# Optimization experiments

Measured on AMD Instinct MI355X. Metric: run time of the kernel, lower is better.

The kernel has to match this reference:

```python
import jax, jax.numpy as jnp
import numpy as np

D = 2        # NUM_DIM (spatial/velocity dimension)
B = 64       # number of (r, r') query pairs
P = 512      # num coefficient positions
NV = 64      # num velocity quadrature points
NC = 1       # num coefficient channels (sigma)
H = 64       # attention MLP hidden width
TW = 128     # transport MLP width
DEPTH = 3    # res_block_depth


def setup_inputs() -> dict:
    key = jax.random.key(0)
    ks = jax.random.split(key, 20)
    rnd = lambda i, shape, s=1.0: (s * jax.random.normal(ks[i], shape, dtype=jnp.float32))
    uni = lambda i, shape: jax.random.uniform(ks[i], shape, dtype=jnp.float32)
    return dict(
        coords=rnd(0, (B, 2 * D)),
        coords_prime=rnd(1, (B, 2 * D)),
        scattering_kernel=uni(2, (B, NV)),
        position_coords=rnd(3, (P, D)),
        sigma=uni(4, (P, NC)),
        velocity_coords=rnd(5, (NV, D)),
        velocity_weights=uni(6, (NV,)),
        self_scattering_kernel=uni(7, (NV, NV)),
        aW0=rnd(8, (2 * D + 2, H), (2 * D + 2) ** -0.5), ab0=jnp.zeros((H,), jnp.float32),
        aW1=rnd(9, (H, H), H ** -0.5), ab1=jnp.zeros((H,), jnp.float32),
        aW2=rnd(10, (H, 1), H ** -0.5), ab2=jnp.zeros((1,), jnp.float32),
        tW0=rnd(11, (4 * D + NC, TW), (4 * D + NC) ** -0.5), tb0=jnp.zeros((TW,), jnp.float32),
        tW1=rnd(12, (TW, TW), TW ** -0.5), tb1=jnp.zeros((TW,), jnp.float32),
        tW2=rnd(13, (TW, TW), TW ** -0.5), tb2=jnp.zeros((TW,), jnp.float32),
        rW=rnd(14, (DEPTH - 1, TW, TW), TW ** -0.5), rb=jnp.zeros((DEPTH - 1, TW), jnp.float32),
        fW=rnd(15, (TW, 1), TW ** -0.5), fb=jnp.zeros((1,), jnp.float32),
    )


def _coeff(x, v, pos, vals, aW0, ab0, aW1, ab1, aW2, ab2):
    # x, v: (..., D); pos: (P, D); vals: (P, NC)
    coords = jnp.concatenate([x, v], axis=-1)                          # (..., 2D)
    ang_g = v / jnp.sqrt(jnp.sum(v * v, axis=-1, keepdims=True) + 1e-16)
    rel = x[..., None, :] - pos                                        # (..., P, D)
    rd = jnp.sqrt(jnp.sum(rel * rel, axis=-1) + 1e-16)                 # (..., P)
    pl = jnp.einsum('...pd,...d->...p', rel, ang_g)                    # positions_local
    al = pl / (rd + 1e-8)                                              # angles_local
    frames = jnp.stack([al, pl], axis=-1)                              # (..., P, 2)
    q = jnp.broadcast_to(coords[..., None, :], frames.shape[:-1] + (coords.shape[-1],))
    qk = jnp.concatenate([q, frames], axis=-1)                         # (..., P, 2D+2)
    h = jax.nn.relu(qk @ aW0 + ab0)
    h = jax.nn.relu(h @ aW1 + ab1)
    logits = (h @ aW2 + ab2)[..., 0]                                   # (..., P)
    logits = jnp.where(pl > 0, logits, -1e30)
    attw = jax.nn.softmax(logits, axis=-1)
    attn = jnp.einsum('...p,pc->...c', attw, vals)                     # (..., NC)
    return jnp.exp(-attn)


def _transport(x, v, xp, vp, pos, vals,
               aW0, ab0, aW1, ab1, aW2, ab2, tW0, tb0, tW1, tb1, tW2, tb2):
    coeff = _coeff(x, v, pos, vals, aW0, ab0, aW1, ab1, aW2, ab2)
    inp = jnp.concatenate([x, v, xp, vp, coeff], axis=-1)              # (..., 4D+NC)
    h = jax.nn.relu(inp @ tW0 + tb0)
    h = jax.nn.relu(h @ tW1 + tb1)
    h = jax.nn.relu(h @ tW2 + tb2)                                     # activate_final=True
    return jnp.exp(h)                                                  # (..., TW)


def _forward(coords, coords_prime, scattering_kernel, position_coords, sigma,
             velocity_coords, velocity_weights, self_scattering_kernel,
             aW0, ab0, aW1, ab1, aW2, ab2, tW0, tb0, tW1, tb1, tW2, tb2,
             rW, rb, fW, fb):
    x, v = coords[:, :D], coords[:, D:]
    xp, vp = coords_prime[:, :D], coords_prime[:, D:]
    mlp_p = (aW0, ab0, aW1, ab1, aW2, ab2, tW0, tb0, tW1, tb1, tW2, tb2)
    # direct transport term: (B, TW)
    g = _transport(x, v, xp, vp, position_coords, sigma, *mlp_p)
    # scatter model: vmap over velocity_coords -> (B, NV, TW)
    b = coords.shape[0]
    vB = jnp.broadcast_to(velocity_coords, (b, NV, D))
    xB = jnp.broadcast_to(x[:, None, :], (b, NV, D))
    xpB = jnp.broadcast_to(xp[:, None, :], (b, NV, D))
    vpB = jnp.broadcast_to(vp[:, None, :], (b, NV, D))
    cur = _transport(xB, vB, xpB, vpB, position_coords, sigma, *mlp_p)
    res_w = (1.0 - self_scattering_kernel) * velocity_weights          # (NV, NV)
    outs = [cur]
    for l in range(DEPTH - 1):  # layer_stack with per-layer params
        r = jnp.einsum('ij,bjw->biw', res_w, cur)
        r = jax.nn.relu(r @ rW[l] + rb[l])                             # MLP([TW]), activate_final
        cur = cur + r
        outs.append(cur)
    scat = jnp.stack(outs)                                             # (DEPTH, B, NV, TW)
    w = (1.0 - scattering_kernel) * velocity_weights                   # (B, NV)
    g = g + jnp.einsum('bj,dbjw->bw', w, scat)
    return g @ fW + fb                                                 # (B, 1)


def reference(coords, coords_prime, scattering_kernel, position_coords, sigma,
              velocity_coords, velocity_weights, self_scattering_kernel,
              aW0, ab0, aW1, ab1, aW2, ab2, tW0, tb0, tW1, tb1, tW2, tb2,
              rW, rb, fW, fb):
    return _forward(coords, coords_prime, scattering_kernel, position_coords, sigma,
                    velocity_coords, velocity_weights, self_scattering_kernel,
                    aW0, ab0, aW1, ab1, aW2, ab2, tW0, tb0, tW1, tb1, tW2, tb2,
                    rW, rb, fW, fb)
```

## Files before the change

kernel.cpp:

```cpp
#include <hip/hip_runtime.h>
#include <hip/hip_bf16.h>
#include <math.h>

#define D 2
#define B 64
#define P 512
#define NV 64
#define H 64
#define TW 128
#define NQ (B*NV + B)

typedef short short8 __attribute__((ext_vector_type(8)));
typedef short short4v __attribute__((ext_vector_type(4)));
typedef float f32x4 __attribute__((ext_vector_type(4)));
typedef int   int4v  __attribute__((ext_vector_type(4)));

static __device__ __forceinline__ unsigned short f2bf(float f) {
    unsigned int u = __builtin_bit_cast(unsigned int, f);
    u += 0x7FFFu + ((u >> 16) & 1u);
    return (unsigned short)(u >> 16);
}
static __device__ __forceinline__ unsigned int pk2bf(float a, float b) {
    __hip_bfloat162 h = __float22bfloat162_rn(make_float2(a, b));
    unsigned int u;
    __builtin_memcpy(&u, &h, 4);
    return u;
}

__global__ __launch_bounds__(256, 2) void coeff_kernel(
    const float* __restrict__ coords, const float* __restrict__ vel,
    const float* __restrict__ pos, const float* __restrict__ sigma,
    const float* __restrict__ aW0, const float* __restrict__ ab0,
    const float* __restrict__ aW1, const float* __restrict__ ab1,
    const float* __restrict__ aW2, const float* __restrict__ ab2,
    float* __restrict__ coeff_out)
{
    __shared__ unsigned short s_w1t[64*72];
    __shared__ float2 s_pos[P];
    __shared__ float  s_logit[2*P];

    const int tid  = threadIdx.x;
    const int lane = tid & 63, wid = tid >> 6;
    const int l15 = lane & 15, lg = lane >> 4;
    const int qi   = wid >> 1;
    const int half = wid & 1;
    const int q = blockIdx.x*2 + qi;

    for (int i = tid; i < H*H; i += 256) {
        const int k = i >> 6, n = i & 63;
        s_w1t[n*72 + k] = f2bf(aW1[i]);
    }
    {
        const float4 p4 = ((const float4*)pos)[tid];
        *(float4*)&s_pos[tid*2] = p4;
    }

    float x0, x1, v0, v1;
    {
        int b;
        if (q < B*NV) { b = q >> 6; const int j = q & 63;
            v0 = vel[2*j]; v1 = vel[2*j+1];
        } else { b = q - B*NV;
            v0 = coords[4*b+2]; v1 = coords[4*b+3];
        }
        x0 = coords[4*b]; x1 = coords[4*b+1];
    }
    const float rinv = rsqrtf(v0*v0 + v1*v1 + 1e-16f);
    const float a0 = v0*rinv, a1 = v1*rinv;

    float basev[16], w4v[16], w5v[16];
    #pragma unroll
    for (int jj = 0; jj < 16; ++jj) {
        const int k = lg*8 + (jj & 7) + (jj >> 3)*32;
        basev[jj] = ab0[k] + x0*aW0[k] + x1*aW0[64+k] + v0*aW0[128+k] + v1*aW0[192+k];
        w4v[jj]   = aW0[256+k];
        w5v[jj]   = aW0[320+k];
    }

    f32x4 b1v[4], w2v[4];
    #pragma unroll
    for (int nt = 0; nt < 4; ++nt) {
        const int n0 = nt*16 + lg*4;
        b1v[nt] = *(const f32x4*)&ab1[n0];
        w2v[nt] = *(const f32x4*)&aW2[n0];
    }
    __syncthreads();

    short8 afrag[4][2];
    #pragma unroll
    for (int nt = 0; nt < 4; ++nt)
        #pragma unroll
        for (int ks = 0; ks < 2; ++ks)
            afrag[nt][ks] = *(const short8*)&s_w1t[(nt*16 + l15)*72 + ks*32 + lg*8];

    #pragma unroll
    for (int jj = 0; jj < 16; ++jj)
        asm volatile("" : "+v"(basev[jj]), "+v"(w4v[jj]), "+v"(w5v[jj]));
    #pragma unroll
    for (int nt = 0; nt < 4; ++nt)
        asm volatile("" : "+v"(b1v[nt]), "+v"(w2v[nt]),
                          "+v"(afrag[nt][0]), "+v"(afrag[nt][1]));

    float pl, al;
    {
        const float2 p0v = s_pos[half*256 + l15];
        const float rx = x0 - p0v.x, ry = x1 - p0v.y;
        const float rd = __builtin_amdgcn_sqrtf(rx*rx + ry*ry + 1e-16f);
        pl = rx*a0 + ry*a1;
        al = __fdividef(pl, rd + 1e-8f);
    }
    for (int ps = 0; ps < 16; ++ps) {
        const int prow = half*256 + ps*16 + l15;
        float pln = pl, aln = al;
        if (ps < 15) {
            const float2 nxt = s_pos[prow + 16];
            const float rxn = x0 - nxt.x, ryn = x1 - nxt.y;
            const float rdn = __builtin_amdgcn_sqrtf(rxn*rxn + ryn*ryn + 1e-16f);
            pln = rxn*a0 + ryn*a1;
            aln = __fdividef(pln, rdn + 1e-8f);
        }

        int4v wlo, whi;
        #pragma unroll
        for (int jp = 0; jp < 4; ++jp) {
            const float t0 = fmaxf(fmaf(pl, w5v[2*jp],   fmaf(al, w4v[2*jp],   basev[2*jp])),   0.f);
            const float t1 = fmaxf(fmaf(pl, w5v[2*jp+1], fmaf(al, w4v[2*jp+1], basev[2*jp+1])), 0.f);
            const float u0 = fmaxf(fmaf(pl, w5v[8+2*jp],   fmaf(al, w4v[8+2*jp],   basev[8+2*jp])),   0.f);
            const float u1 = fmaxf(fmaf(pl, w5v[8+2*jp+1], fmaf(al, w4v[8+2*jp+1], basev[8+2*jp+1])), 0.f);
            wlo[jp] = (int)pk2bf(t0, t1);
            whi[jp] = (int)pk2bf(u0, u1);
        }
        const short8 bf0 = __builtin_bit_cast(short8, wlo);
        const short8 bf1 = __builtin_bit_cast(short8, whi);

        float ssum = 0.f;
        #pragma unroll
        for (int nt = 0; nt < 4; ++nt) {
            f32x4 acc = b1v[nt];
            acc = __builtin_amdgcn_mfma_f32_16x16x32_bf16(afrag[nt][0], bf0, acc, 0, 0, 0);
            acc = __builtin_amdgcn_mfma_f32_16x16x32_bf16(afrag[nt][1], bf1, acc, 0, 0, 0);
            ssum += fmaxf(acc[0], 0.f) * w2v[nt][0];
            ssum += fmaxf(acc[1], 0.f) * w2v[nt][1];
            ssum += fmaxf(acc[2], 0.f) * w2v[nt][2];
            ssum += fmaxf(acc[3], 0.f) * w2v[nt][3];
        }
        ssum += __shfl_xor(ssum, 16, 64);
        ssum += __shfl_xor(ssum, 32, 64);
        if (lane < 16) s_logit[qi*512 + prow] = (pl > 0.f) ? ssum : -1e30f;
        pl = pln; al = aln;
    }
    __syncthreads();

    const float* lgb = &s_logit[qi*512];
    const float4 l0 = *(const float4*)&lgb[lane*8];
    const float4 l1 = *(const float4*)&lgb[lane*8 + 4];
    float m = fmaxf(fmaxf(fmaxf(l0.x, l0.y), fmaxf(l0.z, l0.w)),
                    fmaxf(fmaxf(l1.x, l1.y), fmaxf(l1.z, l1.w)));
    #pragma unroll
    for (int o = 32; o > 0; o >>= 1) m = fmaxf(m, __shfl_xor(m, o, 64));

    const float4 g0 = *(const float4*)&sigma[lane*8];
    const float4 g1 = *(const float4*)&sigma[lane*8 + 4];
    float S = 0.f, T = 0.f, e;
    e = __expf(l0.x - m); S += e; T += e*g0.x;
    e = __expf(l0.y - m); S += e; T += e*g0.y;
    e = __expf(l0.z - m); S += e; T += e*g0.z;
    e = __expf(l0.w - m); S += e; T += e*g0.w;
    e = __expf(l1.x - m); S += e; T += e*g1.x;
    e = __expf(l1.y - m); S += e; T += e*g1.y;
    e = __expf(l1.z - m); S += e; T += e*g1.z;
    e = __expf(l1.w - m); S += e; T += e*g1.w;
    #pragma unroll
    for (int o = 32; o > 0; o >>= 1) { S += __shfl_xor(S, o, 64); T += __shfl_xor(T, o, 64); }
    if (lane == 0 && half == 0) coeff_out[q] = __expf(-(T / S));
}

__global__ __launch_bounds__(512) void transport_kernel(
    const float* __restrict__ coords, const float* __restrict__ coordsp,
    const float* __restrict__ vel,
    const float* __restrict__ tW0, const float* __restrict__ tb0,
    const float* __restrict__ tW1, const float* __restrict__ tb1,
    const float* __restrict__ tW2, const float* __restrict__ tb2,
    const float* __restrict__ coeff_ws, float* __restrict__ cur_ws,
    float* __restrict__ g_ws)
{
    __shared__ unsigned short s_w0t[128*40];
    __shared__ unsigned short s_wt[128*136];
    __shared__ unsigned short s_in[64*40];
    __shared__ unsigned short s_ha[64*136];
    __shared__ unsigned short s_hb[64*136];
    __shared__ float s_b[3*128];

    const int tid = threadIdx.x, g = blockIdx.x;
    const int lane = tid & 63, wid = tid >> 6;
    const int wm = wid & 3, wn = wid >> 2;
    const int l15 = lane & 15, lg = lane >> 4;
    const int irow = wm*16 + lg*4;
    const int qbase = g*64;

    for (int i = tid; i < 128*40; i += 512) {
        const int t = i / 40, k = i % 40;
        s_w0t[i] = (k < 9) ? f2bf(tW0[k*TW + t]) : 0;
    }
    for (int i = tid; i < 64*40; i += 512) s_in[i] = 0;
    {
        const int n = tid & 127, u0 = (tid >> 7)*4;
        #pragma unroll
        for (int k8 = 0; k8 < 8; ++k8) {
            const int u = u0 + 16*k8;
            short4v pk;
            #pragma unroll
            for (int c = 0; c < 4; ++c) pk[c] = (short)f2bf(tW1[(u+c)*TW + n]);
            *(short4v*)&s_wt[n*136 + u] = pk;
        }
    }
    if (tid < 128) { s_b[tid] = tb0[tid]; s_b[128+tid] = tb1[tid]; s_b[256+tid] = tb2[tid]; }
    __syncthreads();

    if (tid < 64) {
        const int q = qbase + tid;
        int b; float v0, v1;
        if (q < B*NV) { b = q >> 6; const int j = q & 63;
            v0 = vel[2*j]; v1 = vel[2*j+1];
        } else { b = q - B*NV;
            v0 = coords[4*b+2]; v1 = coords[4*b+3];
        }
        unsigned short* r = &s_in[tid*40];
        r[0] = f2bf(coords[4*b]);   r[1] = f2bf(coords[4*b+1]);
        r[2] = f2bf(v0);            r[3] = f2bf(v1);
        r[4] = f2bf(coordsp[4*b]);  r[5] = f2bf(coordsp[4*b+1]);
        r[6] = f2bf(coordsp[4*b+2]);r[7] = f2bf(coordsp[4*b+3]);
        r[8] = f2bf(coeff_ws[q]);
    }
    __syncthreads();

    {
        const short8 a0 = *(const short8*)&s_in[(wm*16 + l15)*40 + lg*8];
        #pragma unroll
        for (int nt = 0; nt < 4; ++nt) {
            const int col = wn*64 + nt*16 + l15;
            const short8 b0f = *(const short8*)&s_w0t[col*40 + lg*8];
            const float bias = s_b[col];
            f32x4 acc = { bias, bias, bias, bias };
            acc = __builtin_amdgcn_mfma_f32_16x16x32_bf16(a0, b0f, acc, 0, 0, 0);
            #pragma unroll
            for (int rg = 0; rg < 4; ++rg)
                s_ha[(irow + rg)*136 + col] = f2bf(fmaxf(acc[rg], 0.f));
        }
    }
    __syncthreads();

    {
        short8 af[4];
        #pragma unroll
        for (int ks = 0; ks < 4; ++ks)
            af[ks] = *(const short8*)&s_ha[(wm*16 + l15)*136 + ks*32 + lg*8];
        #pragma unroll
        for (int nt = 0; nt < 4; ++nt) {
            const int col = wn*64 + nt*16 + l15;
            const float bias = s_b[128 + col];
            f32x4 acc = { bias, bias, bias, bias };
            #pragma unroll
            for (int ks = 0; ks < 4; ++ks) {
                const short8 bfr = *(const short8*)&s_wt[col*136 + ks*32 + lg*8];
                acc = __builtin_amdgcn_mfma_f32_16x16x32_bf16(af[ks], bfr, acc, 0, 0, 0);
            }
            #pragma unroll
            for (int rg = 0; rg < 4; ++rg)
                s_hb[(irow + rg)*136 + col] = f2bf(fmaxf(acc[rg], 0.f));
        }
    }
    __syncthreads();

    {
        const int n = tid & 127, u0 = (tid >> 7)*4;
        #pragma unroll
        for (int k8 = 0; k8 < 8; ++k8) {
            const int u = u0 + 16*k8;
            short4v pk;
            #pragma unroll
            for (int c = 0; c < 4; ++c) pk[c] = (short)f2bf(tW2[(u+c)*TW + n]);
            *(short4v*)&s_wt[n*136 + u] = pk;
        }
    }
    __syncthreads();

    {
        short8 af[4];
        #pragma unroll
        for (int ks = 0; ks < 4; ++ks)
            af[ks] = *(const short8*)&s_hb[(wm*16 + l15)*136 + ks*32 + lg*8];
        #pragma unroll
        for (int nt = 0; nt < 4; ++nt) {
            const int col = wn*64 + nt*16 + l15;
            const float bias = s_b[256 + col];
            f32x4 acc = { bias, bias, bias, bias };
            #pragma unroll
            for (int ks = 0; ks < 4; ++ks) {
                const short8 bfr = *(const short8*)&s_wt[col*136 + ks*32 + lg*8];
                acc = __builtin_amdgcn_mfma_f32_16x16x32_bf16(af[ks], bfr, acc, 0, 0, 0);
            }
            #pragma unroll
            for (int rg = 0; rg < 4; ++rg) {
                const float o = __expf(fmaxf(acc[rg], 0.f));
                const int q = qbase + irow + rg;
                if (q < B*NV) cur_ws[q*TW + col] = o;
                else          g_ws[(q - B*NV)*TW + col] = o;
            }
        }
    }
}

__global__ __launch_bounds__(512) void scatter_kernel(
    const float* __restrict__ scat_k, const float* __restrict__ vw,
    const float* __restrict__ ssk,
    const float* __restrict__ rW, const float* __restrict__ rb,
    const float* __restrict__ fW, const float* __restrict__ fb,
    const float* __restrict__ cur_ws, const float* __restrict__ g_ws,
    float* __restrict__ out)
{
    __shared__ unsigned short s_At[128*72];
    __shared__ unsigned short s_r[64*136];
    __shared__ unsigned short s_rWt[128*136];
    __shared__ float s_wl[NV];
    __shared__ float s_fin[4*128];
    __shared__ float s_red[2];

    const int tid = threadIdx.x, b = blockIdx.x;
    const int lane = tid & 63, wid = tid >> 6;
    const int wm = wid & 3, wn = wid >> 2;
    const int l15 = lane & 15, lg = lane >> 4;
    const int irow = wm*16 + lg*4;

    if (tid < NV) s_wl[tid] = (1.f - scat_k[b*NV + tid]) * vw[tid];

    {
        const int w = tid & 127, j0 = tid >> 7;
        #pragma unroll
        for (int k = 0; k < 16; ++k) {
            const int j = j0 + 4*k;
            s_At[w*72 + j] = f2bf(cur_ws[(b*NV + j)*TW + w]);
        }
    }

    float areg[4][4], sreg[4][4];
    #pragma unroll
    for (int n = 0; n < 4; ++n) {
        const int wcol = wn*64 + n*16 + l15;
        #pragma unroll
        for (int rg = 0; rg < 4; ++rg) {
            const float v = cur_ws[(b*NV + irow + rg)*TW + wcol];
            areg[n][rg] = v; sreg[n][rg] = v;
        }
    }

    for (int l = 0; l < 2; ++l) {
        {
            const float* rWl = rW + l*TW*TW;
            const int w = tid & 127, u0 = (tid >> 7)*4;
            #pragma unroll
            for (int k = 0; k < 8; ++k) {
                const int u = u0 + 16*k;
                short4v pk;
                #pragma unroll
                for (int c = 0; c < 4; ++c) pk[c] = (short)f2bf(rWl[(u+c)*TW + w]);
                *(short4v*)&s_rWt[w*136 + u] = pk;
            }
        }
        __syncthreads();

        {
            short8 afrag[2];
            const int row = wm*16 + l15;
            #pragma unroll
            for (int ks = 0; ks < 2; ++ks) {
                const int k0 = ks*32 + lg*8;
                #pragma unroll
                for (int j = 0; j < 8; ++j) {
                    const float rv = (1.f - ssk[row*NV + k0 + j]) * vw[k0 + j];
                    afrag[ks][j] = (short)f2bf(rv);
                }
            }
            #pragma unroll
            for (int n = 0; n < 4; ++n) {
                const int col = wn*64 + n*16 + l15;
                f32x4 acc = {0.f, 0.f, 0.f, 0.f};
                #pragma unroll
                for (int ks = 0; ks < 2; ++ks) {
                    const short8 bfr = *(const short8*)&s_At[col*72 + ks*32 + lg*8];
                    acc = __builtin_amdgcn_mfma_f32_16x16x32_bf16(afrag[ks], bfr, acc, 0, 0, 0);
                }
                #pragma unroll
                for (int rg = 0; rg < 4; ++rg)
                    s_r[(irow + rg)*136 + col] = f2bf(acc[rg]);
            }
        }
        __syncthreads();

        {
            short8 af2[4];
            #pragma unroll
            for (int ks = 0; ks < 4; ++ks)
                af2[ks] = *(const short8*)&s_r[(wm*16 + l15)*136 + ks*32 + lg*8];
            #pragma unroll
            for (int n = 0; n < 4; ++n) {
                const int col = wn*64 + n*16 + l15;
                f32x4 acc = {0.f, 0.f, 0.f, 0.f};
                #pragma unroll
                for (int ks = 0; ks < 4; ++ks) {
                    const short8 bfr = *(const short8*)&s_rWt[col*136 + ks*32 + lg*8];
                    acc = __builtin_amdgcn_mfma_f32_16x16x32_bf16(af2[ks], bfr, acc, 0, 0, 0);
                }
                const float rbv = rb[l*TW + col];
                short4v pk;
                #pragma unroll
                for (int rg = 0; rg < 4; ++rg) {
                    areg[n][rg] += fmaxf(acc[rg] + rbv, 0.f);
                    sreg[n][rg] += areg[n][rg];
                    pk[rg] = (short)f2bf(areg[n][rg]);
                }
                *(short4v*)&s_At[col*72 + irow] = pk;
            }
        }
        __syncthreads();
    }

    float p[4];
    #pragma unroll
    for (int n = 0; n < 4; ++n) {
        float acc = 0.f;
        #pragma unroll
        for (int rg = 0; rg < 4; ++rg) acc += s_wl[irow + rg] * sreg[n][rg];
        acc += __shfl_xor(acc, 16, 64);
        acc += __shfl_xor(acc, 32, 64);
        p[n] = acc;
    }
    if (lg == 0) {
        #pragma unroll
        for (int n = 0; n < 4; ++n)
            s_fin[wm*128 + wn*64 + n*16 + l15] = p[n];
    }
    __syncthreads();

    if (tid < 128) {
        const int w = tid;
        const float tot = s_fin[w] + s_fin[128 + w] + s_fin[256 + w] + s_fin[384 + w];
        float pw = (g_ws[b*TW + w] + tot) * fW[w];
        #pragma unroll
        for (int o = 32; o > 0; o >>= 1) pw += __shfl_down(pw, o, 64);
        if ((tid & 63) == 0) s_red[tid >> 6] = pw;
    }
    __syncthreads();
    if (tid == 0) out[b] = s_red[0] + s_red[1] + fb[0];
}

extern "C" void kernel_launch(void* const* d_in, const int* in_sizes, int n_in,
                              void* d_out, int out_size, void* d_ws, size_t ws_size,
                              hipStream_t stream) {
    const float* coords  = (const float*)d_in[0];
    const float* coordsp = (const float*)d_in[1];
    const float* scatk   = (const float*)d_in[2];
    const float* pos     = (const float*)d_in[3];
    const float* sigma   = (const float*)d_in[4];
    const float* vel     = (const float*)d_in[5];
    const float* vw      = (const float*)d_in[6];
    const float* ssk     = (const float*)d_in[7];
    const float* aW0 = (const float*)d_in[8];
    const float* ab0 = (const float*)d_in[9];
    const float* aW1 = (const float*)d_in[10];
    const float* ab1 = (const float*)d_in[11];
    const float* aW2 = (const float*)d_in[12];
    const float* ab2 = (const float*)d_in[13];
    const float* tW0 = (const float*)d_in[14];
    const float* tb0 = (const float*)d_in[15];
    const float* tW1 = (const float*)d_in[16];
    const float* tb1 = (const float*)d_in[17];
    const float* tW2 = (const float*)d_in[18];
    const float* tb2 = (const float*)d_in[19];
    const float* rW  = (const float*)d_in[20];
    const float* rb  = (const float*)d_in[21];
    const float* fW  = (const float*)d_in[22];
    const float* fb  = (const float*)d_in[23];
    float* out = (float*)d_out;

    float* ws = (float*)d_ws;
    float* coeff_ws = ws;
    float* cur_ws   = ws + 4224;
    float* g_ws     = cur_ws + B*NV*TW;

    hipLaunchKernelGGL(coeff_kernel, dim3(NQ/2), dim3(256), 0, stream,
        coords, vel, pos, sigma, aW0, ab0, aW1, ab1, aW2, ab2, coeff_ws);
    hipLaunchKernelGGL(transport_kernel, dim3(NQ/64), dim3(512), 0, stream,
        coords, coordsp, vel, tW0, tb0, tW1, tb1, tW2, tb2, coeff_ws, cur_ws, g_ws);
    hipLaunchKernelGGL(scatter_kernel, dim3(B), dim3(512), 0, stream,
        scatk, vw, ssk, rW, rb, fW, fb, cur_ws, g_ws, out);
}
```

Baseline: 69.56 us.

## Switch coeff attention MLP to 32x32x16 MFMA and move per-lane constants to LDS

Recasts the attention MLP hidden layer from 16x16x32 to 32x32x16 bf16 MFMA tiles, processing 32 positions per step and halving loop iterations. Per-lane first-layer weights, biases and output weights now live in shared memory and are reloaded each iteration instead of being held in registers. Launch bounds rise to 3 blocks per SM to exploit the lower register pressure. The trade-off is extra LDS traffic in the inner loop and an additional block-wide sync.

```diff
diff --git a/kernel.cpp b/kernel.cpp
--- a/kernel.cpp
+++ b/kernel.cpp
@@ -13,6 +13,7 @@
 typedef short short8 __attribute__((ext_vector_type(8)));
 typedef short short4v __attribute__((ext_vector_type(4)));
 typedef float f32x4 __attribute__((ext_vector_type(4)));
+typedef float f32x16 __attribute__((ext_vector_type(16)));
 typedef int   int4v  __attribute__((ext_vector_type(4)));
 
 static __device__ __forceinline__ unsigned short f2bf(float f) {
@@ -27,7 +28,7 @@
     return u;
 }
 
-__global__ __launch_bounds__(256, 2) void coeff_kernel(
+__global__ __launch_bounds__(256, 3) void coeff_kernel(
     const float* __restrict__ coords, const float* __restrict__ vel,
     const float* __restrict__ pos, const float* __restrict__ sigma,
     const float* __restrict__ aW0, const float* __restrict__ ab0,
@@ -38,10 +39,12 @@
     __shared__ unsigned short s_w1t[64*72];
     __shared__ float2 s_pos[P];
     __shared__ float  s_logit[2*P];
+    __shared__ float  s_cw[4*64];
+    __shared__ float  s_base[2][64];
 
     const int tid  = threadIdx.x;
     const int lane = tid & 63, wid = tid >> 6;
-    const int l15 = lane & 15, lg = lane >> 4;
+    const int l31 = lane & 31, lh = lane >> 5;
     const int qi   = wid >> 1;
     const int half = wid & 1;
     const int q = blockIdx.x*2 + qi;
@@ -54,6 +57,10 @@
         const float4 p4 = ((const float4*)pos)[tid];
         *(float4*)&s_pos[tid*2] = p4;
     }
+    if (tid < 64)        s_cw[tid] = aW0[256 + tid];
+    else if (tid < 128)  s_cw[tid] = aW0[320 + (tid-64)];
+    else if (tid < 192)  s_cw[tid] = ab1[tid-128];
+    else                 s_cw[tid] = aW2[tid-192];
 
     float x0, x1, v0, v1;
     {
@@ -68,85 +75,96 @@
     const float rinv = rsqrtf(v0*v0 + v1*v1 + 1e-16f);
     const float a0 = v0*rinv, a1 = v1*rinv;
 
-    float basev[16], w4v[16], w5v[16];
+    if (half == 0) {
+        const int k = lane;
+        s_base[qi][k] = ab0[k] + x0*aW0[k] + x1*aW0[64+k]
+                      + v0*aW0[128+k] + v1*aW0[192+k];
+    }
+    __syncthreads();
+
+    short8 afrag[2][4];
     #pragma unroll
-    for (int jj = 0; jj < 16; ++jj) {
-        const int k = lg*8 + (jj & 7) + (jj >> 3)*32;
-        basev[jj] = ab0[k] + x0*aW0[k] + x1*aW0[64+k] + v0*aW0[128+k] + v1*aW0[192+k];
-        w4v[jj]   = aW0[256+k];
-        w5v[jj]   = aW0[320+k];
-    }
-
-    f32x4 b1v[4], w2v[4];
+    for (int nt = 0; nt < 2; ++nt)
+        #pragma unroll
+        for (int ks = 0; ks < 4; ++ks)
+            afrag[nt][ks] = *(const short8*)&s_w1t[(nt*32 + l31)*72 + ks*16 + lh*8];
     #pragma unroll
-    for (int nt = 0; nt < 4; ++nt) {
-        const int n0 = nt*16 + lg*4;
-        b1v[nt] = *(const f32x4*)&ab1[n0];
-        w2v[nt] = *(const f32x4*)&aW2[n0];
-    }
-    __syncthreads();
-
-    short8 afrag[4][2];
-    #pragma unroll
-    for (int nt = 0; nt < 4; ++nt)
-        #pragma unroll
-        for (int ks = 0; ks < 2; ++ks)
-            afrag[nt][ks] = *(const short8*)&s_w1t[(nt*16 + l15)*72 + ks*32 + lg*8];
-
-    #pragma unroll
-    for (int jj = 0; jj < 16; ++jj)
-        asm volatile("" : "+v"(basev[jj]), "+v"(w4v[jj]), "+v"(w5v[jj]));
-    #pragma unroll
-    for (int nt = 0; nt < 4; ++nt)
-        asm volatile("" : "+v"(b1v[nt]), "+v"(w2v[nt]),
-                          "+v"(afrag[nt][0]), "+v"(afrag[nt][1]));
+    for (int nt = 0; nt < 2; ++nt)
+        asm volatile("" : "+v"(afrag[nt][0]), "+v"(afrag[nt][1]),
+                          "+v"(afrag[nt][2]), "+v"(afrag[nt][3]));
+
+    const float* bq = s_base[qi];
+    const int k0 = lh*8;
 
     float pl, al;
     {
-        const float2 p0v = s_pos[half*256 + l15];
+        const float2 p0v = s_pos[half*256 + l31];
         const float rx = x0 - p0v.x, ry = x1 - p0v.y;
         const float rd = __builtin_amdgcn_sqrtf(rx*rx + ry*ry + 1e-16f);
         pl = rx*a0 + ry*a1;
         al = __fdividef(pl, rd + 1e-8f);
     }
-    for (int ps = 0; ps < 16; ++ps) {
-        const int prow = half*256 + ps*16 + l15;
+    for (int ps = 0; ps < 8; ++ps) {
+        const int prow = half*256 + ps*32 + l31;
         float pln = pl, aln = al;
-        if (ps < 15) {
-            const float2 nxt = s_pos[prow + 16];
+        if (ps < 7) {
+            const float2 nxt = s_pos[prow + 32];
             const float rxn = x0 - nxt.x, ryn = x1 - nxt.y;
             const float rdn = __builtin_amdgcn_sqrtf(rxn*rxn + ryn*ryn + 1e-16f);
             pln = rxn*a0 + ryn*a1;
             aln = __fdividef(pln, rdn + 1e-8f);
         }
 
-        int4v wlo, whi;
-        #pragma unroll
-        for (int jp = 0; jp < 4; ++jp) {
-            const float t0 = fmaxf(fmaf(pl, w5v[2*jp],   fmaf(al, w4v[2*jp],   basev[2*jp])),   0.f);
-            const float t1 = fmaxf(fmaf(pl, w5v[2*jp+1], fmaf(al, w4v[2*jp+1], basev[2*jp+1])), 0.f);
-            const float u0 = fmaxf(fmaf(pl, w5v[8+2*jp],   fmaf(al, w4v[8+2*jp],   basev[8+2*jp])),   0.f);
-            const float u1 = fmaxf(fmaf(pl, w5v[8+2*jp+1], fmaf(al, w4v[8+2*jp+1], basev[8+2*jp+1])), 0.f);
-            wlo[jp] = (int)pk2bf(t0, t1);
-            whi[jp] = (int)pk2bf(u0, u1);
-        }
-        const short8 bf0 = __builtin_bit_cast(short8, wlo);
-        const short8 bf1 = __builtin_bit_cast(short8, whi);
+        short8 bf[4];
+        #pragma unroll
+        for (int ks = 0; ks < 4; ++ks) {
+            const int kk = ks*16 + k0;
+            const f32x4 w4a = *(const f32x4*)&s_cw[kk];
+            const f32x4 w4b = *(const f32x4*)&s_cw[kk+4];
+            const f32x4 w5a = *(const f32x4*)&s_cw[64+kk];
+            const f32x4 w5b = *(const f32x4*)&s_cw[64+kk+4];
+            const f32x4 ba  = *(const f32x4*)&bq[kk];
+            const f32x4 bb  = *(const f32x4*)&bq[kk+4];
+            f32x4 ra, rb;
+            #pragma unroll
+            for (int c = 0; c < 4; ++c) {
+                ra[c] = fmaxf(fmaf(pl, w5a[c], fmaf(al, w4a[c], ba[c])), 0.f);
+                rb[c] = fmaxf(fmaf(pl, w5b[c], fmaf(al, w4b[c], bb[c])), 0.f);
+            }
+            int4v bi;
+            bi[0] = (int)pk2bf(ra[0], ra[1]);
+            bi[1] = (int)pk2bf(ra[2], ra[3]);
+            bi[2] = (int)pk2bf(rb[0], rb[1]);
+            bi[3] = (int)pk2bf(rb[2], rb[3]);
+            bf[ks] = __builtin_bit_cast(short8, bi);
+        }
 
         float ssum = 0.f;
         #pragma unroll
-        for (int nt = 0; nt < 4; ++nt) {
-            f32x4 acc = b1v[nt];
-            acc = __builtin_amdgcn_mfma_f32_16x16x32_bf16(afrag[nt][0], bf0, acc, 0, 0, 0);
-            acc = __builtin_amdgcn_mfma_f32_16x16x32_bf16(afrag[nt][1], bf1, acc, 0, 0, 0);
-            ssum += fmaxf(acc[0], 0.f) * w2v[nt][0];
-            ssum += fmaxf(acc[1], 0.f) * w2v[nt][1];
-            ssum += fmaxf(acc[2], 0.f) * w2v[nt][2];
-            ssum += fmaxf(acc[3], 0.f) * w2v[nt][3];
-        }
-        ssum += __shfl_xor(ssum, 16, 64);
+        for (int nt = 0; nt < 2; ++nt) {
+            f32x16 acc;
+            #pragma unroll
+            for (int rq = 0; rq < 4; ++rq) {
+                const f32x4 b1x = *(const f32x4*)&s_cw[128 + nt*32 + 8*rq + 4*lh];
+                acc[4*rq]   = b1x[0];
+                acc[4*rq+1] = b1x[1];
+                acc[4*rq+2] = b1x[2];
+                acc[4*rq+3] = b1x[3];
+            }
+            #pragma unroll
+            for (int ks = 0; ks < 4; ++ks)
+                acc = __builtin_amdgcn_mfma_f32_32x32x16_bf16(afrag[nt][ks], bf[ks], acc, 0, 0, 0);
+            #pragma unroll
+            for (int rq = 0; rq < 4; ++rq) {
+                const f32x4 w2x = *(const f32x4*)&s_cw[192 + nt*32 + 8*rq + 4*lh];
+                ssum += fmaxf(acc[4*rq],   0.f) * w2x[0];
+                ssum += fmaxf(acc[4*rq+1], 0.f) * w2x[1];
+                ssum += fmaxf(acc[4*rq+2], 0.f) * w2x[2];
+                ssum += fmaxf(acc[4*rq+3], 0.f) * w2x[3];
+            }
+        }
         ssum += __shfl_xor(ssum, 32, 64);
-        if (lane < 16) s_logit[qi*512 + prow] = (pl > 0.f) ? ssum : -1e30f;
+        if (lane < 32) s_logit[qi*512 + prow] = (pl > 0.f) ? ssum : -1e30f;
         pl = pln; al = aln;
     }
     __syncthreads();
```

Measured after the change: 271.1 us. +289.8%, slower.
